# Optimization experiments

Measured on AMD Instinct MI355X. Metric: run time of the kernel, lower is better.

The kernel has to match this reference:

```python
import jax, jax.numpy as jnp
import numpy as np

N = 100000      # num nodes
E = 1600000     # num edges (avg degree 16)
NFEAT = 128
HID = 128       # eachdim
K = 3           # layer_num (propagation hops)
EPS = 1e-12     # F.normalize eps


def setup_inputs() -> dict:
    key = jax.random.key(0)
    k1, k2, k3, k4 = jax.random.split(key, 4)
    h = jax.random.normal(k1, (N, NFEAT), dtype=jnp.float32)
    edge_index = jax.random.randint(k2, (2, E), 0, N, dtype=jnp.int32)
    W = jax.random.normal(k3, (K + 1, HID, NFEAT), dtype=jnp.float32) * 0.05
    b = jax.random.normal(k4, (K + 1, HID), dtype=jnp.float32) * 0.05
    return {"h": h, "edge_index": edge_index, "Norm": 1, "W": W, "b": b}


def _gcn_norm(edge_index, num_nodes, dtype):
    # PyG gcn_norm with add_self_loops=True, edge_weight=None (all ones)
    loop = jnp.arange(num_nodes, dtype=edge_index.dtype)
    row = jnp.concatenate([edge_index[0], loop])   # source j
    col = jnp.concatenate([edge_index[1], loop])   # target i
    w = jnp.ones(row.shape[0], dtype=dtype)
    deg = jax.ops.segment_sum(w, col, num_segments=num_nodes)
    dinv = jnp.where(deg > 0, jax.lax.rsqrt(deg), 0.0).astype(dtype)
    norm = dinv[row] * dinv[col]                   # [E+N]
    return row, col, norm


def _l2norm_rows(x):
    n = jnp.sqrt(jnp.sum(x * x, axis=1, keepdims=True))
    return x / jnp.maximum(n, EPS)


def reference(h, edge_index, Norm, W, b):
    num_nodes = h.shape[0]
    row, col, norm = _gcn_norm(edge_index, num_nodes, h.dtype)
    # K-hop propagation: out[i] = sum_{j->i} norm_e * x[j]
    mats = [h]
    x = h
    for _ in range(K):
        x = jax.ops.segment_sum(x[row] * norm[:, None], col, num_segments=num_nodes)
        mats.append(x)
    outs = []
    for k, mat in enumerate(mats):
        t = jnp.einsum('nf,hf->nh', mat, W[k]) + b[k]
        if Norm == 1:
            t = _l2norm_rows(t)
        outs.append(t)
    return jnp.concatenate(outs, axis=1)  # [N, (K+1)*HID]
```

## Files before the change

### kernel.cpp

```cpp
#include <hip/hip_runtime.h>

typedef unsigned int uint;
typedef unsigned short ushort;
typedef __attribute__((ext_vector_type(8))) short bf16x8;
typedef __attribute__((ext_vector_type(4))) float f32x4;

__device__ __forceinline__ ushort f2b(float f) {
  uint u = __float_as_uint(f);
  return (ushort)((u + 0x7fffu + ((u >> 16) & 1u)) >> 16);
}
__device__ __forceinline__ uint pk2(float lo, float hi) {
  return (uint)f2b(lo) | ((uint)f2b(hi) << 16);
}
__device__ __forceinline__ void ub2(uint u, float& lo, float& hi) {
  lo = __uint_as_float(u << 16);
  hi = __uint_as_float(u & 0xffff0000u);
}


__global__ __launch_bounds__(256) void k_bcount(const int* __restrict__ col,
                                                int* __restrict__ G, int E, int C) {
  __shared__ int cnt[256];
  cnt[threadIdx.x] = 0;
  __syncthreads();
  int e0 = blockIdx.x * C, e1 = min(E, e0 + C);
  for (int e = e0 + threadIdx.x; e < e1; e += 256)
    atomicAdd(&cnt[__builtin_nontemporal_load(col + e) >> 9], 1);
  __syncthreads();
  G[blockIdx.x * 256 + threadIdx.x] = cnt[threadIdx.x];
}

__global__ __launch_bounds__(256) void k_bscan(const int* __restrict__ G,
                                               int* __restrict__ OFF,
                                               int* __restrict__ bstart, int E) {
  const int b = threadIdx.x;
  int tot = 0;
  for (int blk = 0; blk < 256; ++blk) tot += G[blk * 256 + b];
  __shared__ int s[256];
  s[b] = tot;
  __syncthreads();
  for (int off = 1; off < 256; off <<= 1) {
    int v = s[b];
    int a = (b >= off) ? s[b - off] : 0;
    __syncthreads();
    s[b] = v + a;
    __syncthreads();
  }
  int start = (b > 0) ? s[b - 1] : 0;
  bstart[b] = start;
  if (b == 255) bstart[256] = s[255];
  int run = start;
  for (int blk = 0; blk < 256; ++blk) {
    OFF[blk * 256 + b] = run;
    run += G[blk * 256 + b];
  }
}

__global__ __launch_bounds__(256) void k_bstage(const int* __restrict__ row,
                                                const int* __restrict__ col,
                                                const int* __restrict__ OFF,
                                                int* __restrict__ stag, int E, int C) {
  __shared__ int cur[256];
  cur[threadIdx.x] = OFF[blockIdx.x * 256 + threadIdx.x];
  __syncthreads();
  int e0 = blockIdx.x * C, e1 = min(E, e0 + C);
  for (int e = e0 + threadIdx.x; e < e1; e += 256) {
    int r = __builtin_nontemporal_load(row + e);
    int c = __builtin_nontemporal_load(col + e);
    int pos = atomicAdd(&cur[c >> 9], 1);
    stag[pos] = (r << 9) | (c & 511);
  }
}

__global__ __launch_bounds__(256) void k_bcsr(const int* __restrict__ stag,
                                              const int* __restrict__ bstart,
                                              int* __restrict__ colptr,
                                              int* __restrict__ csr, int N, int E) {
  __shared__ int ldeg[512];
  __shared__ int sd[256];
  const int t = threadIdx.x;
  const int b = blockIdx.x;
  const int c0 = b << 9;
  const int nn = min(512, N - c0);
  const int estart = bstart[b], eend = bstart[b + 1];
  ldeg[t] = 0;
  ldeg[t + 256] = 0;
  __syncthreads();
  for (int i = estart + t; i < eend; i += 256)
    atomicAdd(&ldeg[stag[i] & 511], 1);
  __syncthreads();
  int v0 = ldeg[2 * t], v1 = ldeg[2 * t + 1];
  sd[t] = v0 + v1;
  __syncthreads();
  for (int off = 1; off < 256; off <<= 1) {
    int v = sd[t];
    int a = (t >= off) ? sd[t - off] : 0;
    __syncthreads();
    sd[t] = v + a;
    __syncthreads();
  }
  int a0 = estart + ((t > 0) ? sd[t - 1] : 0);
  int a1 = a0 + v0;
  __syncthreads();
  ldeg[2 * t] = a0;
  ldeg[2 * t + 1] = a1;
  if (2 * t < nn) colptr[c0 + 2 * t] = a0;
  if (2 * t + 1 < nn) colptr[c0 + 2 * t + 1] = a1;
  if (t == 0 && c0 + nn == N) colptr[N] = E;
  __syncthreads();
  for (int i = estart + t; i < eend; i += 256) {
    int pk = stag[i];
    int pos = atomicAdd(&ldeg[pk & 511], 1);
    csr[pos] = pk >> 9;
  }
}

__global__ void k_dinv_cp(const int* __restrict__ colptr, float* __restrict__ dinv,
                          float* __restrict__ sdeg, int N) {
  int i = blockIdx.x * blockDim.x + threadIdx.x;
  if (i < N) {
    float d = (float)(colptr[i + 1] - colptr[i] + 1);
    dinv[i] = rsqrtf(d);
    sdeg[i] = sqrtf(d);
  }
}

__global__ void k_f2b(const float* __restrict__ in, ushort* __restrict__ o, int n8) {
  int i = blockIdx.x * blockDim.x + threadIdx.x;
  if (i >= n8) return;
  const float4* p = (const float4*)(in + (size_t)i * 8);
  float4 A = p[0], B = p[1];
  uint4 u;
  u.x = pk2(A.x, A.y);
  u.y = pk2(A.z, A.w);
  u.z = pk2(B.x, B.y);
  u.w = pk2(B.z, B.w);
  ((uint4*)o)[i] = u;
}

__device__ __forceinline__ void proj_tail(
    const ushort* ylds, float* ssl, float* otile,
    const ushort* __restrict__ wk, const float* __restrict__ biask,
    const float* __restrict__ sdeg, int donorm, float* __restrict__ out,
    int nbase, int koff, int N, int ost, int tid) {
  const int wave = tid >> 6;
  const int lane = tid & 63;
  const int l15 = lane & 15, lhi = lane >> 4;
  f32x4 acc0 = (f32x4)0.f, acc1 = (f32x4)0.f;
  const ushort* ap = ylds + l15 * 136 + lhi * 8;
  const ushort* b0p = wk + ((wave * 32 + l15) << 7) + lhi * 8;
  const ushort* b1p = b0p + (16 << 7);
#pragma unroll
  for (int kk = 0; kk < 4; ++kk) {
    bf16x8 a = *(const bf16x8*)(ap + kk * 32);
    bf16x8 b0 = *(const bf16x8*)(b0p + kk * 32);
    bf16x8 b1 = *(const bf16x8*)(b1p + kk * 32);
    acc0 = __builtin_amdgcn_mfma_f32_16x16x32_bf16(a, b0, acc0, 0, 0, 0);
    acc1 = __builtin_amdgcn_mfma_f32_16x16x32_bf16(a, b1, acc1, 0, 0, 0);
  }
  float s[4];
#pragma unroll
  for (int r = 0; r < 4; ++r) {
    int rg = nbase + lhi * 4 + r;
    s[r] = sdeg[rg < N ? rg : N - 1];
  }
  float bv0 = biask[wave * 32 + l15];
  float bv1 = biask[wave * 32 + 16 + l15];
  float ps[4];
#pragma unroll
  for (int r = 0; r < 4; ++r) {
    acc0[r] = acc0[r] * s[r] + bv0;
    acc1[r] = acc1[r] * s[r] + bv1;
    ps[r] = acc0[r] * acc0[r] + acc1[r] * acc1[r];
  }
#pragma unroll
  for (int m = 1; m < 16; m <<= 1) {
#pragma unroll
    for (int r = 0; r < 4; ++r) ps[r] += __shfl_xor(ps[r], m, 64);
  }
  if (l15 == 0) {
#pragma unroll
    for (int r = 0; r < 4; ++r) ssl[wave * 16 + lhi * 4 + r] = ps[r];
  }
  __syncthreads();
  float sc[4];
#pragma unroll
  for (int r = 0; r < 4; ++r) {
    int rl = lhi * 4 + r;
    float tot = ssl[rl] + ssl[16 + rl] + ssl[32 + rl] + ssl[48 + rl];
    sc[r] = (donorm == 1) ? 1.0f / fmaxf(sqrtf(tot), 1e-12f) : 1.0f;
  }
#pragma unroll
  for (int r = 0; r < 4; ++r) {
    int rl = lhi * 4 + r;
    otile[rl * 132 + wave * 32 + l15] = acc0[r] * sc[r];
    otile[rl * 132 + wave * 32 + 16 + l15] = acc1[r] * sc[r];
  }
  __syncthreads();
#pragma unroll
  for (int i = 0; i < 2; ++i) {
    int idx = tid + 256 * i;
    int rr = idx >> 5, q = idx & 31;
    if (nbase + rr < N) {
      f32x4 vv = *(const f32x4*)&otile[rr * 132 + q * 4];
      __builtin_nontemporal_store(
          vv, (f32x4*)(out + (size_t)(nbase + rr) * ost + koff + q * 4));
    }
  }
}

__device__ __forceinline__ void add8(uint4 v, float& a0, float& a1, float& a2, float& a3,
                                     float& a4, float& a5, float& a6, float& a7) {
  float t0, t1;
  ub2(v.x, t0, t1); a0 += t0; a1 += t1;
  ub2(v.y, t0, t1); a2 += t0; a3 += t1;
  ub2(v.z, t0, t1); a4 += t0; a5 += t1;
  ub2(v.w, t0, t1); a6 += t0; a7 += t1;
}

__global__ __launch_bounds__(256) void k_hopproj(
    const ushort* __restrict__ xin, ushort* __restrict__ yout,
    const ushort* __restrict__ wk, const float* __restrict__ biask,
    const float* __restrict__ sdeg, const float* __restrict__ dinv,
    const int* __restrict__ colptr, const int* __restrict__ csr,
    const int* __restrict__ normp, float* __restrict__ out,
    int koff, int N, int ost, int writeY) {
  __shared__ ushort ylds[16 * 136];
  __shared__ float ssl[64];
  __shared__ float otile[16 * 132];
  const int tid = threadIdx.x;
  const int nbase = blockIdx.x * 16;
  const int node = nbase + (tid >> 4);
  const int g = tid & 15;
  const int nc = node < N ? node : N - 1;

  float di = dinv[nc];
  float w2 = di * di;
  uint4 v = ((const uint4*)(xin + (size_t)nc * 128))[g];
  float a0, a1, a2, a3, a4, a5, a6, a7;
  ub2(v.x, a0, a1); ub2(v.y, a2, a3); ub2(v.z, a4, a5); ub2(v.w, a6, a7);

  int p = colptr[nc], p1 = colptr[nc + 1];
  for (; p + 4 <= p1; p += 4) {
    int s0 = __builtin_nontemporal_load(csr + p);
    int s1 = __builtin_nontemporal_load(csr + p + 1);
    int s2 = __builtin_nontemporal_load(csr + p + 2);
    int s3 = __builtin_nontemporal_load(csr + p + 3);
    uint4 x0 = ((const uint4*)(xin + (size_t)s0 * 128))[g];
    uint4 x1 = ((const uint4*)(xin + (size_t)s1 * 128))[g];
    uint4 x2 = ((const uint4*)(xin + (size_t)s2 * 128))[g];
    uint4 x3 = ((const uint4*)(xin + (size_t)s3 * 128))[g];
    add8(x0, a0, a1, a2, a3, a4, a5, a6, a7);
    add8(x1, a0, a1, a2, a3, a4, a5, a6, a7);
    add8(x2, a0, a1, a2, a3, a4, a5, a6, a7);
    add8(x3, a0, a1, a2, a3, a4, a5, a6, a7);
  }
  for (; p < p1; ++p) {
    int s0 = __builtin_nontemporal_load(csr + p);
    uint4 x0 = ((const uint4*)(xin + (size_t)s0 * 128))[g];
    add8(x0, a0, a1, a2, a3, a4, a5, a6, a7);
  }
  uint4 o;
  o.x = pk2(w2 * a0, w2 * a1);
  o.y = pk2(w2 * a2, w2 * a3);
  o.z = pk2(w2 * a4, w2 * a5);
  o.w = pk2(w2 * a6, w2 * a7);
  if (writeY && node < N) ((uint4*)(yout + (size_t)node * 128))[g] = o;
  *(uint4*)(ylds + (tid >> 4) * 136 + g * 8) = o;
  __syncthreads();

  proj_tail(ylds, ssl, otile, wk, biask, sdeg, normp[0], out, nbase, koff, N,
            ost, tid);
}

__global__ __launch_bounds__(256) void k_y0proj(
    const float* __restrict__ h, ushort* __restrict__ yout,
    const ushort* __restrict__ wk, const float* __restrict__ biask,
    const float* __restrict__ sdeg, const float* __restrict__ dinv,
    const int* __restrict__ normp, float* __restrict__ out, int N, int ost) {
  __shared__ ushort ylds[16 * 136];
  __shared__ float ssl[64];
  __shared__ float otile[16 * 132];
  const int tid = threadIdx.x;
  const int nbase = blockIdx.x * 16;
  const int node = nbase + (tid >> 4);
  const int g = tid & 15;
  const int nc = node < N ? node : N - 1;

  float d = dinv[nc];
  const float4* p = (const float4*)(h + (size_t)nc * 128 + g * 8);
  float4 A = p[0], B = p[1];
  uint4 o;
  o.x = pk2(A.x * d, A.y * d);
  o.y = pk2(A.z * d, A.w * d);
  o.z = pk2(B.x * d, B.y * d);
  o.w = pk2(B.z * d, B.w * d);
  ((uint4*)(yout + (size_t)nc * 128))[g] = o;
  *(uint4*)(ylds + (tid >> 4) * 136 + g * 8) = o;
  __syncthreads();

  proj_tail(ylds, ssl, otile, wk, biask, sdeg, normp[0], out, nbase, 0, N, ost,
            tid);
}

__global__ void k_zero(uint4* __restrict__ p, int n4) {
  int stride = gridDim.x * blockDim.x;
  for (int i = blockIdx.x * blockDim.x + threadIdx.x; i < n4; i += stride)
    p[i] = make_uint4(0, 0, 0, 0);
}

__global__ void k_deg(const int* __restrict__ col, int* __restrict__ deg, int E) {
  int i = blockIdx.x * blockDim.x + threadIdx.x;
  if (i < E) atomicAdd(&deg[col[i]], 1);
}

__global__ void k_dinv_deg(const int* __restrict__ deg, float* __restrict__ dinv,
                           float* __restrict__ sdeg, int N) {
  int i = blockIdx.x * blockDim.x + threadIdx.x;
  if (i < N) {
    float d = (float)(deg[i] + 1);
    dinv[i] = rsqrtf(d);
    sdeg[i] = sqrtf(d);
  }
}

__global__ void k_scan1(const int* __restrict__ deg, int* __restrict__ colptr,
                        int* __restrict__ part, int N) {
  __shared__ int sd[256];
  int t = threadIdx.x;
  int base = blockIdx.x * 1024 + t * 4;
  int v0 = base + 0 < N ? deg[base + 0] : 0;
  int v1 = base + 1 < N ? deg[base + 1] : 0;
  int v2 = base + 2 < N ? deg[base + 2] : 0;
  int v3 = base + 3 < N ? deg[base + 3] : 0;
  sd[t] = v0 + v1 + v2 + v3;
  __syncthreads();
  for (int off = 1; off < 256; off <<= 1) {
    int val = sd[t];
    int add = (t >= off) ? sd[t - off] : 0;
    __syncthreads();
    sd[t] = val + add;
    __syncthreads();
  }
  int excl = (t > 0) ? sd[t - 1] : 0;
  if (t == 255) part[blockIdx.x] = sd[255];
  if (base + 0 < N) colptr[base + 0] = excl;
  if (base + 1 < N) colptr[base + 1] = excl + v0;
  if (base + 2 < N) colptr[base + 2] = excl + v0 + v1;
  if (base + 3 < N) colptr[base + 3] = excl + v0 + v1 + v2;
}

__global__ void k_scan2(int* __restrict__ part, int nb) {
  __shared__ int sd[1024];
  int t = threadIdx.x;
  sd[t] = (t < nb) ? part[t] : 0;
  __syncthreads();
  for (int off = 1; off < 1024; off <<= 1) {
    int val = sd[t];
    int add = (t >= off) ? sd[t - off] : 0;
    __syncthreads();
    sd[t] = val + add;
    __syncthreads();
  }
  if (t < nb) part[t] = (t > 0) ? sd[t - 1] : 0;
}

__global__ void k_scan3(int* __restrict__ colptr, const int* __restrict__ part, int N, int E) {
  int i = blockIdx.x * blockDim.x + threadIdx.x;
  if (i < N) colptr[i] += part[i >> 10];
  if (i == 0) colptr[N] = E;
}

__global__ void k_fill(const int* __restrict__ row, const int* __restrict__ col,
                       const int* __restrict__ colptr, int* __restrict__ cursor,
                       const float* __restrict__ dinv, int2* __restrict__ csr, int E) {
  int stride = gridDim.x * blockDim.x;
  for (int i = blockIdx.x * blockDim.x + threadIdx.x; i < E; i += stride) {
    int r = row[i], c = col[i];
    int pos = colptr[c] + atomicAdd(&cursor[c], 1);
    int2 v;
    v.x = r;
    v.y = __float_as_int(dinv[r] * dinv[c]);
    csr[pos] = v;
  }
}

__global__ void k_wt(const float* __restrict__ W, float* __restrict__ Wt, int total) {
  int i = blockIdx.x * blockDim.x + threadIdx.x;
  if (i < total) {
    int k = i >> 14, rem = i & 16383, h = rem >> 7, f = rem & 127;
    Wt[(k << 14) + f * 128 + h] = W[i];
  }
}

__global__ __launch_bounds__(256) void k_hop(
    const float* __restrict__ xsrc, int xstride,
    float* __restrict__ out, int dst_off, int ost,
    const int* __restrict__ colptr, const int2* __restrict__ csr,
    const float* __restrict__ dinv, int N) {
  int gid = blockIdx.x * blockDim.x + threadIdx.x;
  int node = gid >> 5, lane = gid & 31;
  if (node >= N) return;
  float di = dinv[node];
  float4 acc = *(const float4*)(xsrc + (size_t)node * xstride + lane * 4);
  float w = di * di;
  acc.x *= w; acc.y *= w; acc.z *= w; acc.w *= w;
  int p1 = colptr[node + 1];
  for (int p = colptr[node]; p < p1; ++p) {
    int2 ev = csr[p];
    float v = __int_as_float(ev.y);
    float4 x = *(const float4*)(xsrc + (size_t)ev.x * xstride + lane * 4);
    acc.x += v * x.x; acc.y += v * x.y; acc.z += v * x.z; acc.w += v * x.w;
  }
  *(float4*)(out + (size_t)node * ost + dst_off + lane * 4) = acc;
}

__global__ __launch_bounds__(256) void k_gemm(
    const float* __restrict__ h, const float* __restrict__ Wt_g,
    const float* __restrict__ bias, const int* __restrict__ normp,
    float* __restrict__ out, int N, int ost) {
  __shared__ float Wt[128 * 128];
  __shared__ float xl[32 * 128];
  const int k = blockIdx.y;
  const int row0 = blockIdx.x * 32;
  const int tid = threadIdx.x;
  const float4* Wg4 = (const float4*)(Wt_g + ((size_t)k << 14));
  float4* Wt4 = (float4*)Wt;
#pragma unroll
  for (int i = 0; i < 16; ++i) Wt4[tid + 256 * i] = Wg4[tid + 256 * i];
  const float* xs = (k == 0) ? h : (out + k * 128);
  const int xst = (k == 0) ? 128 : ost;
  float4* xl4 = (float4*)xl;
#pragma unroll
  for (int i = 0; i < 4; ++i) {
    int idx = tid + 256 * i;
    int r = idx >> 5, fq = idx & 31;
    int rg = row0 + r;
    if (rg >= N) rg = N - 1;
    xl4[idx] = *((const float4*)(xs + (size_t)rg * xst) + fq);
  }
  __syncthreads();
  const int hq = tid & 31;
  const int rq = tid >> 5;
  float acc[4][4] = {{0.f}};
  const float* xb = xl + rq * 4 * 128;
#pragma unroll 4
  for (int f = 0; f < 128; ++f) {
    float4 wv = *(const float4*)(Wt + f * 128 + hq * 4);
    float x0 = xb[f];
    float x1 = xb[128 + f];
    float x2 = xb[256 + f];
    float x3 = xb[384 + f];
    acc[0][0] += x0 * wv.x; acc[0][1] += x0 * wv.y; acc[0][2] += x0 * wv.z; acc[0][3] += x0 * wv.w;
    acc[1][0] += x1 * wv.x; acc[1][1] += x1 * wv.y; acc[1][2] += x1 * wv.z; acc[1][3] += x1 * wv.w;
    acc[2][0] += x2 * wv.x; acc[2][1] += x2 * wv.y; acc[2][2] += x2 * wv.z; acc[2][3] += x2 * wv.w;
    acc[3][0] += x3 * wv.x; acc[3][1] += x3 * wv.y; acc[3][2] += x3 * wv.z; acc[3][3] += x3 * wv.w;
  }
  float4 bv = *((const float4*)(bias + (size_t)k * 128) + hq);
#pragma unroll
  for (int rl = 0; rl < 4; ++rl) {
    acc[rl][0] += bv.x; acc[rl][1] += bv.y; acc[rl][2] += bv.z; acc[rl][3] += bv.w;
  }
  float ss[4];
#pragma unroll
  for (int rl = 0; rl < 4; ++rl)
    ss[rl] = acc[rl][0] * acc[rl][0] + acc[rl][1] * acc[rl][1] +
             acc[rl][2] * acc[rl][2] + acc[rl][3] * acc[rl][3];
#pragma unroll
  for (int m = 1; m < 32; m <<= 1) {
#pragma unroll
    for (int rl = 0; rl < 4; ++rl) ss[rl] += __shfl_xor(ss[rl], m, 64);
  }
  const int donorm = normp[0];
#pragma unroll
  for (int rl = 0; rl < 4; ++rl) {
    float sc = 1.0f;
    if (donorm == 1) sc = 1.0f / fmaxf(sqrtf(ss[rl]), 1e-12f);
    int rg = row0 + rq * 4 + rl;
    if (rg < N) {
      float4 oo;
      oo.x = acc[rl][0] * sc; oo.y = acc[rl][1] * sc;
      oo.z = acc[rl][2] * sc; oo.w = acc[rl][3] * sc;
      *((float4*)(out + (size_t)rg * ost + k * 128) + hq) = oo;
    }
  }
}

extern "C" void kernel_launch(void* const* d_in, const int* in_sizes, int n_in,
                              void* d_out, int out_size, void* d_ws, size_t ws_size,
                              hipStream_t stream) {
  const float* h = (const float*)d_in[0];
  const int* ei = (const int*)d_in[1];
  const int* normp = (const int*)d_in[2];
  const float* W = (const float*)d_in[3];
  const float* bias = (const float*)d_in[4];
  float* out = (float*)d_out;

  const int N = in_sizes[0] / 128;
  const int E = in_sizes[1] / 2;
  const int KP1 = in_sizes[3] / (128 * 128);
  const int OST = KP1 * 128;
  const int* row = ei;
  const int* col = ei + E;

  char* ws = (char*)d_ws;
  size_t used = 0;
  auto carve = [&](size_t bytes) {
    char* p = ws + used;
    used += (bytes + 255) & ~(size_t)255;
    return p;
  };
  int* colptr = (int*)carve((size_t)(N + 1) * 4);
  float* dinv = (float*)carve((size_t)N * 4);
  float* sdeg = (float*)carve((size_t)N * 4);

  const size_t al = 255;
  const size_t bucketable = (size_t)N <= 131072 ? 1 : 0;
  const size_t gB = 256 * 256 * 4;
  const size_t needBf = used + 2 * ((gB + al) & ~al) + 4096 +
                        2 * (((size_t)E * 4 + al) & ~al) +
                        (((size_t)KP1 * 128 * 128 * 2 + al) & ~al) +
                        2 * (((size_t)N * 128 * 2 + al) & ~al);

  if (bucketable && ws_size >= needBf) {
    int* G = (int*)carve(gB);
    int* OFF = (int*)carve(gB);
    int* bstart = (int*)carve(4096);
    int* stag = (int*)carve((size_t)E * 4);
    int* csr = (int*)carve((size_t)E * 4);
    ushort* Wb = (ushort*)carve((size_t)KP1 * 128 * 128 * 2);
    ushort* bufA = (ushort*)carve((size_t)N * 128 * 2);
    ushort* bufB = (ushort*)carve((size_t)N * 128 * 2);

    const int C = (E + 255) / 256;
    const int NBUK = (N + 511) >> 9;
    const int nblk = (N + 255) / 256;

    k_bcount<<<256, 256, 0, stream>>>(col, G, E, C);
    k_bscan<<<1, 256, 0, stream>>>(G, OFF, bstart, E);
    k_bstage<<<256, 256, 0, stream>>>(row, col, OFF, stag, E, C);
    k_bcsr<<<NBUK, 256, 0, stream>>>(stag, bstart, colptr, csr, N, E);
    k_dinv_cp<<<nblk, 256, 0, stream>>>(colptr, dinv, sdeg, N);
    k_f2b<<<(KP1 * 2048 + 255) / 256, 256, 0, stream>>>(W, Wb, KP1 * 2048);

    int gb = (N + 15) / 16;
    k_y0proj<<<gb, 256, 0, stream>>>(h, bufA, Wb, bias, sdeg, dinv, normp, out,
                                     N, OST);
    ushort* cur = bufA;
    ushort* nxt = bufB;
    for (int kk = 1; kk < KP1; ++kk) {
      k_hopproj<<<gb, 256, 0, stream>>>(
          cur, nxt, Wb + (kk << 14), bias + kk * 128, sdeg, dinv, colptr, csr,
          normp, out, kk * 128, N, OST, (kk < KP1 - 1) ? 1 : 0);
      ushort* t = cur; cur = nxt; nxt = t;
    }
  } else {
    int* deg = (int*)carve((size_t)N * 4);
    int* part = (int*)carve(4096);
    int* cursor = (int*)carve((size_t)N * 4);
    int2* csr2 = (int2*)carve((size_t)E * 8);
    float* Wt_g = (float*)carve((size_t)KP1 * 128 * 128 * 4);
    const int eb = (E + 255) / 256;
    const int nblk = (N + 255) / 256;
    k_zero<<<32, 256, 0, stream>>>((uint4*)deg, (N + 3) / 4);
    k_zero<<<32, 256, 0, stream>>>((uint4*)cursor, (N + 3) / 4);
    k_deg<<<eb, 256, 0, stream>>>(col, deg, E);
    k_dinv_deg<<<nblk, 256, 0, stream>>>(deg, dinv, sdeg, N);
    int nb = (N + 1023) / 1024;
    k_scan1<<<nb, 256, 0, stream>>>(deg, colptr, part, N);
    k_scan2<<<1, 1024, 0, stream>>>(part, nb);
    k_scan3<<<nblk, 256, 0, stream>>>(colptr, part, N, E);
    k_fill<<<1024, 256, 0, stream>>>(row, col, colptr, cursor, dinv, csr2, E);
    k_wt<<<(KP1 * 16384 + 255) / 256, 256, 0, stream>>>(W, Wt_g, KP1 * 16384);
    int hopBlocks = (N * 32 + 255) / 256;
    for (int kk = 1; kk < KP1; ++kk) {
      const float* src = (kk == 1) ? h : (out + (kk - 1) * 128);
      int st = (kk == 1) ? 128 : OST;
      k_hop<<<hopBlocks, 256, 0, stream>>>(src, st, out, kk * 128, OST,
                                           colptr, csr2, dinv, N);
    }
    k_gemm<<<dim3((N + 31) / 32, KP1), 256, 0, stream>>>(h, Wt_g, bias, normp,
                                                         out, N, OST);
  }
}
```

Baseline: 370.4 us.

## Process 32 nodes per block with 8 lanes per node in gather and projection

The hop-propagation and y0 kernels now handle 32 nodes per 256-thread block, with 8 threads per node each loading two 16-byte chunks per neighbour instead of 16 threads loading one. This gives more independent gathers in flight per thread and halves the block count. The projection tail is called twice per block, so the weight tile is reused across two 16-row tiles, at the cost of an extra barrier and more registers per thread. The output write loop is also manually unrolled.

```diff
diff --git a/kernel.cpp b/kernel.cpp
--- a/kernel.cpp
+++ b/kernel.cpp
@@ -16,7 +16,6 @@
   lo = __uint_as_float(u << 16);
   hi = __uint_as_float(u & 0xffff0000u);
 }
-
 
 __global__ __launch_bounds__(256) void k_bcount(const int* __restrict__ col,
                                                 int* __restrict__ G, int E, int C) {
@@ -197,25 +196,30 @@
     otile[rl * 132 + wave * 32 + 16 + l15] = acc1[r] * sc[r];
   }
   __syncthreads();
-#pragma unroll
-  for (int i = 0; i < 2; ++i) {
-    int idx = tid + 256 * i;
-    int rr = idx >> 5, q = idx & 31;
-    if (nbase + rr < N) {
+  {
+    int rr = tid >> 5, q = tid & 31;
+    if (rr < 16 && nbase + rr < N) {
       f32x4 vv = *(const f32x4*)&otile[rr * 132 + q * 4];
       __builtin_nontemporal_store(
           vv, (f32x4*)(out + (size_t)(nbase + rr) * ost + koff + q * 4));
     }
-  }
-}
-
-__device__ __forceinline__ void add8(uint4 v, float& a0, float& a1, float& a2, float& a3,
-                                     float& a4, float& a5, float& a6, float& a7) {
+    int idx = tid + 256;
+    rr = idx >> 5;
+    q = idx & 31;
+    if (rr < 16 && nbase + rr < N) {
+      f32x4 vv = *(const f32x4*)&otile[rr * 132 + q * 4];
+      __builtin_nontemporal_store(
+          vv, (f32x4*)(out + (size_t)(nbase + rr) * ost + koff + q * 4));
+    }
+  }
+}
+
+__device__ __forceinline__ void add8(uint4 v, float* a) {
   float t0, t1;
-  ub2(v.x, t0, t1); a0 += t0; a1 += t1;
-  ub2(v.y, t0, t1); a2 += t0; a3 += t1;
-  ub2(v.z, t0, t1); a4 += t0; a5 += t1;
-  ub2(v.w, t0, t1); a6 += t0; a7 += t1;
+  ub2(v.x, t0, t1); a[0] += t0; a[1] += t1;
+  ub2(v.y, t0, t1); a[2] += t0; a[3] += t1;
+  ub2(v.z, t0, t1); a[4] += t0; a[5] += t1;
+  ub2(v.w, t0, t1); a[6] += t0; a[7] += t1;
 }
 
 __global__ __launch_bounds__(256) void k_hopproj(
@@ -225,20 +229,33 @@
     const int* __restrict__ colptr, const int* __restrict__ csr,
     const int* __restrict__ normp, float* __restrict__ out,
     int koff, int N, int ost, int writeY) {
-  __shared__ ushort ylds[16 * 136];
+  __shared__ ushort ylds[32 * 136];
   __shared__ float ssl[64];
   __shared__ float otile[16 * 132];
   const int tid = threadIdx.x;
-  const int nbase = blockIdx.x * 16;
-  const int node = nbase + (tid >> 4);
-  const int g = tid & 15;
+  const int grp = tid >> 3;
+  const int l = tid & 7;
+  const int nbase = blockIdx.x * 32;
+  const int node = nbase + grp;
   const int nc = node < N ? node : N - 1;
 
   float di = dinv[nc];
   float w2 = di * di;
-  uint4 v = ((const uint4*)(xin + (size_t)nc * 128))[g];
-  float a0, a1, a2, a3, a4, a5, a6, a7;
-  ub2(v.x, a0, a1); ub2(v.y, a2, a3); ub2(v.z, a4, a5); ub2(v.w, a6, a7);
+  const ushort* xrow = xin + (size_t)nc * 128;
+  uint4 vA = *(const uint4*)(xrow + l * 8);
+  uint4 vB = *(const uint4*)(xrow + 64 + l * 8);
+  float aA[8], aB[8];
+  {
+    float t0, t1;
+    ub2(vA.x, t0, t1); aA[0] = t0; aA[1] = t1;
+    ub2(vA.y, t0, t1); aA[2] = t0; aA[3] = t1;
+    ub2(vA.z, t0, t1); aA[4] = t0; aA[5] = t1;
+    ub2(vA.w, t0, t1); aA[6] = t0; aA[7] = t1;
+    ub2(vB.x, t0, t1); aB[0] = t0; aB[1] = t1;
+    ub2(vB.y, t0, t1); aB[2] = t0; aB[3] = t1;
+    ub2(vB.z, t0, t1); aB[4] = t0; aB[5] = t1;
+    ub2(vB.w, t0, t1); aB[6] = t0; aB[7] = t1;
+  }
 
   int p = colptr[nc], p1 = colptr[nc + 1];
   for (; p + 4 <= p1; p += 4) {
@@ -246,31 +263,54 @@
     int s1 = __builtin_nontemporal_load(csr + p + 1);
     int s2 = __builtin_nontemporal_load(csr + p + 2);
     int s3 = __builtin_nontemporal_load(csr + p + 3);
-    uint4 x0 = ((const uint4*)(xin + (size_t)s0 * 128))[g];
-    uint4 x1 = ((const uint4*)(xin + (size_t)s1 * 128))[g];
-    uint4 x2 = ((const uint4*)(xin + (size_t)s2 * 128))[g];
-    uint4 x3 = ((const uint4*)(xin + (size_t)s3 * 128))[g];
-    add8(x0, a0, a1, a2, a3, a4, a5, a6, a7);
-    add8(x1, a0, a1, a2, a3, a4, a5, a6, a7);
-    add8(x2, a0, a1, a2, a3, a4, a5, a6, a7);
-    add8(x3, a0, a1, a2, a3, a4, a5, a6, a7);
+    const ushort* r0 = xin + (size_t)s0 * 128;
+    const ushort* r1 = xin + (size_t)s1 * 128;
+    const ushort* r2 = xin + (size_t)s2 * 128;
+    const ushort* r3 = xin + (size_t)s3 * 128;
+    uint4 xA0 = *(const uint4*)(r0 + l * 8);
+    uint4 xB0 = *(const uint4*)(r0 + 64 + l * 8);
+    uint4 xA1 = *(const uint4*)(r1 + l * 8);
+    uint4 xB1 = *(const uint4*)(r1 + 64 + l * 8);
+    uint4 xA2 = *(const uint4*)(r2 + l * 8);
+    uint4 xB2 = *(const uint4*)(r2 + 64 + l * 8);
+    uint4 xA3 = *(const uint4*)(r3 + l * 8);
+    uint4 xB3 = *(const uint4*)(r3 + 64 + l * 8);
+    add8(xA0, aA); add8(xB0, aB);
+    add8(xA1, aA); add8(xB1, aB);
+    add8(xA2, aA); add8(xB2, aB);
+    add8(xA3, aA); add8(xB3, aB);
   }
   for (; p < p1; ++p) {
     int s0 = __builtin_nontemporal_load(csr + p);
-    uint4 x0 = ((const uint4*)(xin + (size_t)s0 * 128))[g];
-    add8(x0, a0, a1, a2, a3, a4, a5, a6, a7);
-  }
-  uint4 o;
-  o.x = pk2(w2 * a0, w2 * a1);
-  o.y = pk2(w2 * a2, w2 * a3);
-  o.z = pk2(w2 * a4, w2 * a5);
-  o.w = pk2(w2 * a6, w2 * a7);
-  if (writeY && node < N) ((uint4*)(yout + (size_t)node * 128))[g] = o;
-  *(uint4*)(ylds + (tid >> 4) * 136 + g * 8) = o;
-  __syncthreads();
-
-  proj_tail(ylds, ssl, otile, wk, biask, sdeg, normp[0], out, nbase, koff, N,
+    const ushort* r0 = xin + (size_t)s0 * 128;
+    uint4 xA0 = *(const uint4*)(r0 + l * 8);
+    uint4 xB0 = *(const uint4*)(r0 + 64 + l * 8);
+    add8(xA0, aA); add8(xB0, aB);
+  }
+  uint4 oA, oB;
+  oA.x = pk2(w2 * aA[0], w2 * aA[1]);
+  oA.y = pk2(w2 * aA[2], w2 * aA[3]);
+  oA.z = pk2(w2 * aA[4], w2 * aA[5]);
+  oA.w = pk2(w2 * aA[6], w2 * aA[7]);
+  oB.x = pk2(w2 * aB[0], w2 * aB[1]);
+  oB.y = pk2(w2 * aB[2], w2 * aB[3]);
+  oB.z = pk2(w2 * aB[4], w2 * aB[5]);
+  oB.w = pk2(w2 * aB[6], w2 * aB[7]);
+  if (writeY && node < N) {
+    ushort* yrow = yout + (size_t)node * 128;
+    *(uint4*)(yrow + l * 8) = oA;
+    *(uint4*)(yrow + 64 + l * 8) = oB;
+  }
+  *(uint4*)(ylds + grp * 136 + l * 8) = oA;
+  *(uint4*)(ylds + grp * 136 + 64 + l * 8) = oB;
+  __syncthreads();
+
+  const int donorm = normp[0];
+  proj_tail(ylds, ssl, otile, wk, biask, sdeg, donorm, out, nbase, koff, N,
             ost, tid);
+  __syncthreads();
+  proj_tail(ylds + 16 * 136, ssl, otile, wk, biask, sdeg, donorm, out,
+            nbase + 16, koff, N, ost, tid);
 }
 
 __global__ __launch_bounds__(256) void k_y0proj(
@@ -278,29 +318,37 @@
     const ushort* __restrict__ wk, const float* __restrict__ biask,
     const float* __restrict__ sdeg, const float* __restrict__ dinv,
     const int* __restrict__ normp, float* __restrict__ out, int N, int ost) {
-  __shared__ ushort ylds[16 * 136];
+  __shared__ ushort ylds[32 * 136];
   __shared__ float ssl[64];
   __shared__ float otile[16 * 132];
   const int tid = threadIdx.x;
-  const int nbase = blockIdx.x * 16;
-  const int node = nbase + (tid >> 4);
-  const int g = tid & 15;
+  const int grp = tid >> 3;
+  const int l = tid & 7;
+  const int nbase = blockIdx.x * 32;
+  const int node = nbase + grp;
   const int nc = node < N ? node : N - 1;
 
   float d = dinv[nc];
-  const float4* p = (const float4*)(h + (size_t)nc * 128 + g * 8);
-  float4 A = p[0], B = p[1];
-  uint4 o;
-  o.x = pk2(A.x * d, A.y * d);
-  o.y = pk2(A.z * d, A.w * d);
-  o.z = pk2(B.x * d, B.y * d);
-  o.w = pk2(B.z * d, B.w * d);
-  ((uint4*)(yout + (size_t)nc * 128))[g] = o;
-  *(uint4*)(ylds + (tid >> 4) * 136 + g * 8) = o;
-  __syncthreads();
-
-  proj_tail(ylds, ssl, otile, wk, biask, sdeg, normp[0], out, nbase, 0, N, ost,
+  const float* hrow = h + (size_t)nc * 128;
+#pragma unroll
+  for (int chunk = 0; chunk < 4; ++chunk) {
+    int d0 = chunk * 32 + l * 4;
+    float4 f = *(const float4*)(hrow + d0);
+    uint2 u;
+    u.x = pk2(f.x * d, f.y * d);
+    u.y = pk2(f.z * d, f.w * d);
+    *(uint2*)(ylds + grp * 136 + d0) = u;
+    ushort* yrow = yout + (size_t)nc * 128;
+    *(uint2*)(yrow + d0) = u;
+  }
+  __syncthreads();
+
+  const int donorm = normp[0];
+  proj_tail(ylds, ssl, otile, wk, biask, sdeg, donorm, out, nbase, 0, N, ost,
             tid);
+  __syncthreads();
+  proj_tail(ylds + 16 * 136, ssl, otile, wk, biask, sdeg, donorm, out,
+            nbase + 16, 0, N, ost, tid);
 }
 
 __global__ void k_zero(uint4* __restrict__ p, int n4) {
@@ -543,7 +591,7 @@
     k_dinv_cp<<<nblk, 256, 0, stream>>>(colptr, dinv, sdeg, N);
     k_f2b<<<(KP1 * 2048 + 255) / 256, 256, 0, stream>>>(W, Wb, KP1 * 2048);
 
-    int gb = (N + 15) / 16;
+    int gb = (N + 31) / 32;
     k_y0proj<<<gb, 256, 0, stream>>>(h, bufA, Wb, bias, sdeg, dinv, normp, out,
                                      N, OST);
     ushort* cur = bufA;
```

Result: slower. 392.6 us (+6.0%).
